# Kernel optimization log

Hardware: AMD Instinct MI355X
Metric: run time of the kernel (lower is better)

The kernel has to match this reference:

```python
import jax, jax.numpy as jnp
import numpy as np

TEMPERATURE = 0.1
BASE_TEMPERATURE = 0.07
N = 8192
D = 128


def setup_inputs() -> dict:
    key = jax.random.key(0)
    kf, kl = jax.random.split(key)
    feats = jax.random.normal(kf, (N, 1, D), dtype=jnp.float32)
    # contrastive embeddings are typically L2-normalized upstream
    feats = feats / jnp.linalg.norm(feats, axis=-1, keepdims=True)
    labels = jax.random.randint(kl, (N,), 0, 2, dtype=jnp.int32)
    return {"feats": feats, "labels": labels}


def reference(feats, labels):
    # feats: [anchor_num, n_view=1, D]; labels: [anchor_num] binary fg/bg
    anchor_num, n_view, d = feats.shape
    n = anchor_num * n_view  # n_view == 1 in this module
    contrast_feature = feats.reshape(n, d)

    lab = labels.reshape(-1, 1)
    pos_mask = (lab == lab.T).astype(feats.dtype)  # [N, N]
    neg_mask = 1.0 - pos_mask

    # [N, N] similarity logits
    logits = jnp.matmul(contrast_feature, contrast_feature.T) / TEMPERATURE
    logits_max = jax.lax.stop_gradient(jnp.max(logits, axis=1, keepdims=True))
    logits = logits - logits_max

    # mask out self-contrast on the diagonal (logits_mask in torch code)
    idx = jnp.arange(n)
    pos_mask = pos_mask.at[idx, idx].set(0.0)

    exp_logits = jnp.exp(logits)
    neg_logits = jnp.sum(exp_logits * neg_mask, axis=1, keepdims=True)  # [N,1]
    log_prob = logits - jnp.log(exp_logits + neg_logits)

    mean_log_prob_pos = jnp.sum(pos_mask * log_prob, axis=1) / jnp.sum(pos_mask, axis=1)
    loss = -(TEMPERATURE / BASE_TEMPERATURE) * mean_log_prob_pos
    return jnp.mean(loss)
```

## Files before the change

### kernel.cpp

```cpp
#include <hip/hip_runtime.h>
#include <hip/hip_bf16.h>

#define NN 8192
#define DD 128

typedef short bf16x8 __attribute__((ext_vector_type(8)));
typedef float f32x4 __attribute__((ext_vector_type(4)));

#define CSCALE  3.7982829f
#define SLSCALE 2.6327684f

#define LABF_OFF (NN * DD * 2)
#define G_OFF    (LABF_OFF + NN * 4)
#define CNT_OFF  (G_OFF + 1024)
#define CTR2_OFF (G_OFF + 1028)
#define ACC_OFF  (G_OFF + 1032)
#define CTR_OFF  (G_OFF + 1152)
#define EG_OFF   (G_OFF + 1280)
#define ELG_OFF  (EG_OFF + NN * 4)

#define BROWS 256
#define BCOLS 512
#define TCOLS 32
#define ITERS (BCOLS / TCOLS)

__device__ __forceinline__ unsigned short f2bf(float x) {
    unsigned u = __float_as_uint(x);
    u = (u + 0x7FFFu + ((u >> 16) & 1u)) >> 16;
    return (unsigned short)u;
}

__global__ __launch_bounds__(256) void prep_kernel(const float* __restrict__ F,
        const int* __restrict__ labels, unsigned short* __restrict__ F16,
        float* __restrict__ labf, float* __restrict__ G,
        int* __restrict__ cnt1, float* __restrict__ Eg, float* __restrict__ Elg) {
    __shared__ float sG[256];
    __shared__ int scnt;
    const int tid = threadIdx.x;
    sG[tid] = 0.f;
    if (tid == 0) scnt = 0;
    __syncthreads();
    const int wave = tid >> 6, lane = tid & 63;
    const int half = lane >> 5, l32 = lane & 31;
    const int rb = blockIdx.x * 32;
    if (tid < 32) { Eg[rb + tid] = 0.f; Elg[rb + tid] = 0.f; }
    int mycnt = 0;
    float g1a[4] = {0.f, 0.f, 0.f, 0.f}, gta[4] = {0.f, 0.f, 0.f, 0.f};
    #pragma unroll
    for (int it = 0; it < 4; ++it) {
        const int row = rb + it * 8 + wave * 2 + half;
        const int lab = labels[row];
        const float lf = (float)lab;
        const float4 f = *reinterpret_cast<const float4*>(F + row * DD + l32 * 4);
        ushort4 u;
        u.x = f2bf(CSCALE * f.x); u.y = f2bf(CSCALE * f.y);
        u.z = f2bf(CSCALE * f.z); u.w = f2bf(CSCALE * f.w);
        *reinterpret_cast<ushort4*>(F16 + row * DD + l32 * 4) = u;
        g1a[0] = fmaf(lf, f.x, g1a[0]); gta[0] += f.x;
        g1a[1] = fmaf(lf, f.y, g1a[1]); gta[1] += f.y;
        g1a[2] = fmaf(lf, f.z, g1a[2]); gta[2] += f.z;
        g1a[3] = fmaf(lf, f.w, g1a[3]); gta[3] += f.w;
        if (l32 == 0) {
            labf[row] = lf;
            mycnt += lab;
        }
    }
    #pragma unroll
    for (int j = 0; j < 4; ++j) {
        atomicAdd(&sG[l32 * 4 + j], g1a[j]);
        atomicAdd(&sG[128 + l32 * 4 + j], gta[j]);
    }
    if (l32 == 0 && mycnt) atomicAdd(&scnt, mycnt);
    __syncthreads();
    atomicAdd(&G[tid], sG[tid]);
    if (tid == 0) atomicAdd(cnt1, scnt);
}

__global__ __launch_bounds__(256, 2) void loss_kernel(
        const unsigned short* __restrict__ F16, const float* __restrict__ labf,
        const int* __restrict__ labels, const float* __restrict__ G,
        const int* __restrict__ cnt1, float* __restrict__ Eg,
        float* __restrict__ Elg, int* __restrict__ ctr, int* __restrict__ ctr2,
        float* __restrict__ acc, float* __restrict__ out) {
    __shared__ unsigned short Bt[2][TCOLS * DD];
    __shared__ float Lab[BCOLS];
    __shared__ int sLast;
    __shared__ float wsum[4];
    const int tid  = threadIdx.x;
    const int wave = tid >> 6, lane = tid & 63;
    const int quad = lane >> 4, l16 = lane & 15;
    const int rb = (blockIdx.x & 31) * BROWS;
    const int cb = (blockIdx.x >> 5) * BCOLS;

    Lab[tid]       = labf[cb + tid];
    Lab[tid + 256] = labf[cb + tid + 256];

    const int rw = rb + wave * 64;
    bf16x8 a[4][4];
    #pragma unroll
    for (int m = 0; m < 4; m++)
        #pragma unroll
        for (int kb = 0; kb < 4; kb++)
            a[m][kb] = *reinterpret_cast<const bf16x8*>(
                F16 + (rw + m * 16 + l16) * DD + kb * 32 + quad * 8);

    const int scol = tid >> 3;
    const int sc0  = (tid & 7) * 2;
    const unsigned short* sbase = F16 + (cb + scol) * DD + sc0 * 8;
    const int sdst0 = sc0 * (TCOLS * 8) + (((scol ^ sc0) & 31) * 8);
    const int sdst1 = (sc0 + 1) * (TCOLS * 8) + (((scol ^ (sc0 + 1)) & 31) * 8);

    *reinterpret_cast<bf16x8*>(&Bt[0][sdst0]) =
        *reinterpret_cast<const bf16x8*>(sbase);
    *reinterpret_cast<bf16x8*>(&Bt[0][sdst1]) =
        *reinterpret_cast<const bf16x8*>(sbase + 8);

    float accE[4][4] = {}, accEl[4][4] = {};
    __syncthreads();

    for (int it = 0; it < ITERS; ++it) {
        const int cur = it & 1;
        const int itn = (it + 1) & (ITERS - 1);
        const bf16x8 vn0 = *reinterpret_cast<const bf16x8*>(sbase + itn * TCOLS * DD);
        const bf16x8 vn1 = *reinterpret_cast<const bf16x8*>(sbase + itn * TCOLS * DD + 8);

        #pragma unroll
        for (int g = 0; g < 2; ++g) {
            bf16x8 bfr[4];
            #pragma unroll
            for (int kb = 0; kb < 4; kb++) {
                const int cr = kb * 4 + quad;
                const int col = g * 16 + l16;
                bfr[kb] = *reinterpret_cast<const bf16x8*>(
                    &Bt[cur][cr * (TCOLS * 8) + (((col ^ cr) & 31) * 8)]);
            }
            f32x4 d0 = {0.f, 0.f, 0.f, 0.f}, d1 = {0.f, 0.f, 0.f, 0.f};
            f32x4 d2 = {0.f, 0.f, 0.f, 0.f}, d3 = {0.f, 0.f, 0.f, 0.f};
            #pragma unroll
            for (int kb = 0; kb < 4; kb++) {
                d0 = __builtin_amdgcn_mfma_f32_16x16x32_bf16(a[0][kb], bfr[kb], d0, 0, 0, 0);
                d1 = __builtin_amdgcn_mfma_f32_16x16x32_bf16(a[1][kb], bfr[kb], d1, 0, 0, 0);
                d2 = __builtin_amdgcn_mfma_f32_16x16x32_bf16(a[2][kb], bfr[kb], d2, 0, 0, 0);
                d3 = __builtin_amdgcn_mfma_f32_16x16x32_bf16(a[3][kb], bfr[kb], d3, 0, 0, 0);
            }
            const float lc = Lab[it * TCOLS + g * 16 + l16];
            #pragma unroll
            for (int r = 0; r < 4; r++) {
                const float e0 = exp2f(d0[r]);
                accE[0][r] += e0; accEl[0][r] = fmaf(lc, e0, accEl[0][r]);
                const float e1 = exp2f(d1[r]);
                accE[1][r] += e1; accEl[1][r] = fmaf(lc, e1, accEl[1][r]);
                const float e2 = exp2f(d2[r]);
                accE[2][r] += e2; accEl[2][r] = fmaf(lc, e2, accEl[2][r]);
                const float e3 = exp2f(d3[r]);
                accE[3][r] += e3; accEl[3][r] = fmaf(lc, e3, accEl[3][r]);
            }
        }

        *reinterpret_cast<bf16x8*>(&Bt[cur ^ 1][sdst0]) = vn0;
        *reinterpret_cast<bf16x8*>(&Bt[cur ^ 1][sdst1]) = vn1;
        __syncthreads();
    }

    #pragma unroll
    for (int m = 0; m < 4; m++) {
        #pragma unroll
        for (int r = 0; r < 4; r++) {
            float e = accE[m][r], el = accEl[m][r];
            #pragma unroll
            for (int off = 1; off < 16; off <<= 1) {
                e  += __shfl_xor(e,  off);
                el += __shfl_xor(el, off);
            }
            if (l16 == 0) {
                const int row = rw + m * 16 + quad * 4 + r;
                atomicAdd(&Eg[row], e);
                atomicAdd(&Elg[row], el);
            }
        }
    }

    __syncthreads();
    if (tid == 0) sLast = (atomicAdd(&ctr[blockIdx.x & 31], 1) == 15);
    __syncthreads();
    if (!sLast) return;

    Lab[tid] = G[tid];
    __syncthreads();

    const int row = rb + tid;
    const int lr  = labels[row];
    const float E  = atomicAdd(&Eg[row], 0.f);
    const float El = atomicAdd(&Elg[row], 0.f);
    float dot = 0.f;
    const unsigned short* fp = F16 + row * DD;
    #pragma unroll
    for (int k = 0; k < DD; k += 8) {
        const bf16x8 fv = *reinterpret_cast<const bf16x8*>(fp + k);
        #pragma unroll
        for (int j = 0; j < 8; j++) {
            const float fj = __uint_as_float(((unsigned)(unsigned short)fv[j]) << 16);
            const float g1 = Lab[k + j];
            const float gl = lr ? g1 : (Lab[128 + k + j] - g1);
            dot = fmaf(fj, gl, dot);
        }
    }
    const float Epos = lr ? El : (E - El);
    const float Si   = E - Epos;
    const int   c1   = *cnt1;
    const float cntp1 = (float)(lr ? c1 : (NN - c1));
    const float cntm  = cntp1 - 1.f;
    const float sum_l   = SLSCALE * dot;
    const float sum_log = cntp1 * __logf(Si) + Epos / Si;
    float li = -(10.f / 7.f) * (sum_l - sum_log) / cntm;
    #pragma unroll
    for (int off = 1; off < 64; off <<= 1) li += __shfl_xor(li, off);
    if ((tid & 63) == 0) wsum[tid >> 6] = li;
    __syncthreads();
    if (tid == 0) {
        atomicAdd(acc, (wsum[0] + wsum[1] + wsum[2] + wsum[3]) * (1.0f / NN));
        __threadfence();
        if (atomicAdd(ctr2, 1) == 31) out[0] = atomicAdd(acc, 0.f);
    }
}

extern "C" void kernel_launch(void* const* d_in, const int* in_sizes, int n_in,
                              void* d_out, int out_size, void* d_ws, size_t ws_size,
                              hipStream_t stream) {
    const float* F      = (const float*)d_in[0];
    const int*   labels = (const int*)d_in[1];
    float*       out    = (float*)d_out;
    char*        ws     = (char*)d_ws;
    unsigned short* F16 = (unsigned short*)ws;
    float*       labf   = (float*)(ws + LABF_OFF);
    float*       G      = (float*)(ws + G_OFF);
    int*         cnt1   = (int*)(ws + CNT_OFF);
    int*         ctr2   = (int*)(ws + CTR2_OFF);
    float*       acc    = (float*)(ws + ACC_OFF);
    int*         ctr    = (int*)(ws + CTR_OFF);
    float*       Eg     = (float*)(ws + EG_OFF);
    float*       Elg    = (float*)(ws + ELG_OFF);

    hipMemsetAsync(ws + G_OFF, 0, 1280, stream);

    prep_kernel<<<NN / 32, 256, 0, stream>>>(F, labels, F16, labf, G, cnt1, Eg, Elg);
    loss_kernel<<<512, 256, 0, stream>>>(F16, labf, labels, G, cnt1, Eg, Elg,
                                         ctr, ctr2, acc, out);
}
```

Before: 102.7 us.

## Fuse bf16 prep into loss kernel and accumulate logit sums in-loop

Removes the separate prep kernel. The loss kernel now reads fp32 features directly and converts them to bf16 on the fly for both the A registers and the B tiles in LDS. The per-row positive-logit sum that used to come from a dot with global feature sums is replaced by extra in-loop accumulators of raw logits, and label counts are built per row group with atomics. This saves one launch and the F16 round trip through memory, but doubles global load bytes per tile, adds conversion ALU work and 32 more accumulator registers in the hot loop, and requires memsetting a larger workspace.

```diff
diff --git a/kernel.cpp b/kernel.cpp
--- a/kernel.cpp
+++ b/kernel.cpp
@@ -8,121 +8,104 @@
 typedef float f32x4 __attribute__((ext_vector_type(4)));
 
 #define CSCALE  3.7982829f
-#define SLSCALE 2.6327684f
-
-#define LABF_OFF (NN * DD * 2)
-#define G_OFF    (LABF_OFF + NN * 4)
-#define CNT_OFF  (G_OFF + 1024)
-#define CTR2_OFF (G_OFF + 1028)
-#define ACC_OFF  (G_OFF + 1032)
-#define CTR_OFF  (G_OFF + 1152)
-#define EG_OFF   (G_OFF + 1280)
+#define LN2     0.69314718056f
+
+#define CTR_OFF  0
+#define CTRC_OFF 128
+#define CTR2_OFF 256
+#define ACC_OFF  260
+#define EG_OFF   512
 #define ELG_OFF  (EG_OFF + NN * 4)
+#define SG_OFF   (ELG_OFF + NN * 4)
+#define SLG_OFF  (SG_OFF + NN * 4)
+#define WS_ZERO  (SLG_OFF + NN * 4)
 
 #define BROWS 256
 #define BCOLS 512
 #define TCOLS 32
 #define ITERS (BCOLS / TCOLS)
 
-__device__ __forceinline__ unsigned short f2bf(float x) {
-    unsigned u = __float_as_uint(x);
-    u = (u + 0x7FFFu + ((u >> 16) & 1u)) >> 16;
-    return (unsigned short)u;
+__device__ __forceinline__ bf16x8 cvt8(float4 fa, float4 fb) {
+    union { __hip_bfloat16 h[8]; bf16x8 v; } u;
+    u.h[0] = __float2bfloat16(CSCALE * fa.x);
+    u.h[1] = __float2bfloat16(CSCALE * fa.y);
+    u.h[2] = __float2bfloat16(CSCALE * fa.z);
+    u.h[3] = __float2bfloat16(CSCALE * fa.w);
+    u.h[4] = __float2bfloat16(CSCALE * fb.x);
+    u.h[5] = __float2bfloat16(CSCALE * fb.y);
+    u.h[6] = __float2bfloat16(CSCALE * fb.z);
+    u.h[7] = __float2bfloat16(CSCALE * fb.w);
+    return u.v;
 }
 
-__global__ __launch_bounds__(256) void prep_kernel(const float* __restrict__ F,
-        const int* __restrict__ labels, unsigned short* __restrict__ F16,
-        float* __restrict__ labf, float* __restrict__ G,
-        int* __restrict__ cnt1, float* __restrict__ Eg, float* __restrict__ Elg) {
-    __shared__ float sG[256];
-    __shared__ int scnt;
-    const int tid = threadIdx.x;
-    sG[tid] = 0.f;
-    if (tid == 0) scnt = 0;
-    __syncthreads();
-    const int wave = tid >> 6, lane = tid & 63;
-    const int half = lane >> 5, l32 = lane & 31;
-    const int rb = blockIdx.x * 32;
-    if (tid < 32) { Eg[rb + tid] = 0.f; Elg[rb + tid] = 0.f; }
-    int mycnt = 0;
-    float g1a[4] = {0.f, 0.f, 0.f, 0.f}, gta[4] = {0.f, 0.f, 0.f, 0.f};
-    #pragma unroll
-    for (int it = 0; it < 4; ++it) {
-        const int row = rb + it * 8 + wave * 2 + half;
-        const int lab = labels[row];
-        const float lf = (float)lab;
-        const float4 f = *reinterpret_cast<const float4*>(F + row * DD + l32 * 4);
-        ushort4 u;
-        u.x = f2bf(CSCALE * f.x); u.y = f2bf(CSCALE * f.y);
-        u.z = f2bf(CSCALE * f.z); u.w = f2bf(CSCALE * f.w);
-        *reinterpret_cast<ushort4*>(F16 + row * DD + l32 * 4) = u;
-        g1a[0] = fmaf(lf, f.x, g1a[0]); gta[0] += f.x;
-        g1a[1] = fmaf(lf, f.y, g1a[1]); gta[1] += f.y;
-        g1a[2] = fmaf(lf, f.z, g1a[2]); gta[2] += f.z;
-        g1a[3] = fmaf(lf, f.w, g1a[3]); gta[3] += f.w;
-        if (l32 == 0) {
-            labf[row] = lf;
-            mycnt += lab;
-        }
-    }
-    #pragma unroll
-    for (int j = 0; j < 4; ++j) {
-        atomicAdd(&sG[l32 * 4 + j], g1a[j]);
-        atomicAdd(&sG[128 + l32 * 4 + j], gta[j]);
-    }
-    if (l32 == 0 && mycnt) atomicAdd(&scnt, mycnt);
-    __syncthreads();
-    atomicAdd(&G[tid], sG[tid]);
-    if (tid == 0) atomicAdd(cnt1, scnt);
-}
-
-__global__ __launch_bounds__(256, 2) void loss_kernel(
-        const unsigned short* __restrict__ F16, const float* __restrict__ labf,
-        const int* __restrict__ labels, const float* __restrict__ G,
-        const int* __restrict__ cnt1, float* __restrict__ Eg,
-        float* __restrict__ Elg, int* __restrict__ ctr, int* __restrict__ ctr2,
-        float* __restrict__ acc, float* __restrict__ out) {
+__global__ __launch_bounds__(256, 2) void fused_kernel(
+        const float* __restrict__ F, const int* __restrict__ labels,
+        int* __restrict__ ctr, float* __restrict__ ctrC,
+        int* __restrict__ ctr2, float* __restrict__ acc,
+        float* __restrict__ Eg, float* __restrict__ Elg,
+        float* __restrict__ Sg, float* __restrict__ Slg,
+        float* __restrict__ out) {
     __shared__ unsigned short Bt[2][TCOLS * DD];
     __shared__ float Lab[BCOLS];
     __shared__ int sLast;
     __shared__ float wsum[4];
     const int tid  = threadIdx.x;
+    const int bid  = blockIdx.x;
     const int wave = tid >> 6, lane = tid & 63;
     const int quad = lane >> 4, l16 = lane & 15;
-    const int rb = (blockIdx.x & 31) * BROWS;
-    const int cb = (blockIdx.x >> 5) * BCOLS;
-
-    Lab[tid]       = labf[cb + tid];
-    Lab[tid + 256] = labf[cb + tid + 256];
+    const int rg = bid & 31;
+    const int rb = rg * BROWS;
+    const int cb = (bid >> 5) * BCOLS;
+
+    Lab[tid]       = (float)labels[cb + tid];
+    Lab[tid + 256] = (float)labels[cb + tid + 256];
 
     const int rw = rb + wave * 64;
     bf16x8 a[4][4];
     #pragma unroll
     for (int m = 0; m < 4; m++)
         #pragma unroll
-        for (int kb = 0; kb < 4; kb++)
-            a[m][kb] = *reinterpret_cast<const bf16x8*>(
-                F16 + (rw + m * 16 + l16) * DD + kb * 32 + quad * 8);
+        for (int kb = 0; kb < 4; kb++) {
+            const float* ap = F + (rw + m * 16 + l16) * DD + kb * 32 + quad * 8;
+            const float4 fa = *reinterpret_cast<const float4*>(ap);
+            const float4 fb = *reinterpret_cast<const float4*>(ap + 4);
+            a[m][kb] = cvt8(fa, fb);
+        }
 
     const int scol = tid >> 3;
     const int sc0  = (tid & 7) * 2;
-    const unsigned short* sbase = F16 + (cb + scol) * DD + sc0 * 8;
+    const float* sbaseF = F + (cb + scol) * DD + sc0 * 8;
     const int sdst0 = sc0 * (TCOLS * 8) + (((scol ^ sc0) & 31) * 8);
     const int sdst1 = (sc0 + 1) * (TCOLS * 8) + (((scol ^ (sc0 + 1)) & 31) * 8);
 
-    *reinterpret_cast<bf16x8*>(&Bt[0][sdst0]) =
-        *reinterpret_cast<const bf16x8*>(sbase);
-    *reinterpret_cast<bf16x8*>(&Bt[0][sdst1]) =
-        *reinterpret_cast<const bf16x8*>(sbase + 8);
+    {
+        const float4 va = *reinterpret_cast<const float4*>(sbaseF + 0);
+        const float4 vb = *reinterpret_cast<const float4*>(sbaseF + 4);
+        const float4 vc = *reinterpret_cast<const float4*>(sbaseF + 8);
+        const float4 vd = *reinterpret_cast<const float4*>(sbaseF + 12);
+        *reinterpret_cast<bf16x8*>(&Bt[0][sdst0]) = cvt8(va, vb);
+        *reinterpret_cast<bf16x8*>(&Bt[0][sdst1]) = cvt8(vc, vd);
+    }
 
     float accE[4][4] = {}, accEl[4][4] = {};
-    __syncthreads();
+    float accS[4][4] = {}, accSl[4][4] = {};
+    __syncthreads();
+
+    {
+        float cc = Lab[wave * 64 + lane] + Lab[256 + wave * 64 + lane];
+        #pragma unroll
+        for (int off = 1; off < 64; off <<= 1) cc += __shfl_xor(cc, off);
+        if (lane == 0) atomicAdd(&ctrC[rg], cc);
+    }
 
     for (int it = 0; it < ITERS; ++it) {
         const int cur = it & 1;
         const int itn = (it + 1) & (ITERS - 1);
-        const bf16x8 vn0 = *reinterpret_cast<const bf16x8*>(sbase + itn * TCOLS * DD);
-        const bf16x8 vn1 = *reinterpret_cast<const bf16x8*>(sbase + itn * TCOLS * DD + 8);
+        const float* pf = sbaseF + itn * TCOLS * DD;
+        const float4 va = *reinterpret_cast<const float4*>(pf + 0);
+        const float4 vb = *reinterpret_cast<const float4*>(pf + 4);
+        const float4 vc = *reinterpret_cast<const float4*>(pf + 8);
+        const float4 vd = *reinterpret_cast<const float4*>(pf + 12);
 
         #pragma unroll
         for (int g = 0; g < 2; ++g) {
@@ -148,17 +131,21 @@
             for (int r = 0; r < 4; r++) {
                 const float e0 = exp2f(d0[r]);
                 accE[0][r] += e0; accEl[0][r] = fmaf(lc, e0, accEl[0][r]);
+                accS[0][r] += d0[r]; accSl[0][r] = fmaf(lc, d0[r], accSl[0][r]);
                 const float e1 = exp2f(d1[r]);
                 accE[1][r] += e1; accEl[1][r] = fmaf(lc, e1, accEl[1][r]);
+                accS[1][r] += d1[r]; accSl[1][r] = fmaf(lc, d1[r], accSl[1][r]);
                 const float e2 = exp2f(d2[r]);
                 accE[2][r] += e2; accEl[2][r] = fmaf(lc, e2, accEl[2][r]);
+                accS[2][r] += d2[r]; accSl[2][r] = fmaf(lc, d2[r], accSl[2][r]);
                 const float e3 = exp2f(d3[r]);
                 accE[3][r] += e3; accEl[3][r] = fmaf(lc, e3, accEl[3][r]);
+                accS[3][r] += d3[r]; accSl[3][r] = fmaf(lc, d3[r], accSl[3][r]);
             }
         }
 
-        *reinterpret_cast<bf16x8*>(&Bt[cur ^ 1][sdst0]) = vn0;
-        *reinterpret_cast<bf16x8*>(&Bt[cur ^ 1][sdst1]) = vn1;
+        *reinterpret_cast<bf16x8*>(&Bt[cur ^ 1][sdst0]) = cvt8(va, vb);
+        *reinterpret_cast<bf16x8*>(&Bt[cur ^ 1][sdst1]) = cvt8(vc, vd);
         __syncthreads();
     }
 
@@ -167,50 +154,41 @@
         #pragma unroll
         for (int r = 0; r < 4; r++) {
             float e = accE[m][r], el = accEl[m][r];
+            float s = accS[m][r], sl = accSl[m][r];
             #pragma unroll
             for (int off = 1; off < 16; off <<= 1) {
                 e  += __shfl_xor(e,  off);
                 el += __shfl_xor(el, off);
+                s  += __shfl_xor(s,  off);
+                sl += __shfl_xor(sl, off);
             }
             if (l16 == 0) {
                 const int row = rw + m * 16 + quad * 4 + r;
                 atomicAdd(&Eg[row], e);
                 atomicAdd(&Elg[row], el);
+                atomicAdd(&Sg[row], s);
+                atomicAdd(&Slg[row], sl);
             }
         }
     }
 
     __syncthreads();
-    if (tid == 0) sLast = (atomicAdd(&ctr[blockIdx.x & 31], 1) == 15);
+    if (tid == 0) sLast = (atomicAdd(&ctr[rg], 1) == 15);
     __syncthreads();
     if (!sLast) return;
-
-    Lab[tid] = G[tid];
-    __syncthreads();
 
     const int row = rb + tid;
     const int lr  = labels[row];
-    const float E  = atomicAdd(&Eg[row], 0.f);
-    const float El = atomicAdd(&Elg[row], 0.f);
-    float dot = 0.f;
-    const unsigned short* fp = F16 + row * DD;
-    #pragma unroll
-    for (int k = 0; k < DD; k += 8) {
-        const bf16x8 fv = *reinterpret_cast<const bf16x8*>(fp + k);
-        #pragma unroll
-        for (int j = 0; j < 8; j++) {
-            const float fj = __uint_as_float(((unsigned)(unsigned short)fv[j]) << 16);
-            const float g1 = Lab[k + j];
-            const float gl = lr ? g1 : (Lab[128 + k + j] - g1);
-            dot = fmaf(fj, gl, dot);
-        }
-    }
+    const float E   = atomicAdd(&Eg[row], 0.f);
+    const float El  = atomicAdd(&Elg[row], 0.f);
+    const float S   = atomicAdd(&Sg[row], 0.f);
+    const float Sl  = atomicAdd(&Slg[row], 0.f);
+    const float c1f = atomicAdd(&ctrC[rg], 0.f);
     const float Epos = lr ? El : (E - El);
     const float Si   = E - Epos;
-    const int   c1   = *cnt1;
-    const float cntp1 = (float)(lr ? c1 : (NN - c1));
+    const float cntp1 = lr ? c1f : ((float)NN - c1f);
     const float cntm  = cntp1 - 1.f;
-    const float sum_l   = SLSCALE * dot;
+    const float sum_l   = (lr ? Sl : (S - Sl)) * LN2;
     const float sum_log = cntp1 * __logf(Si) + Epos / Si;
     float li = -(10.f / 7.f) * (sum_l - sum_log) / cntm;
     #pragma unroll
@@ -231,19 +209,17 @@
     const int*   labels = (const int*)d_in[1];
     float*       out    = (float*)d_out;
     char*        ws     = (char*)d_ws;
-    unsigned short* F16 = (unsigned short*)ws;
-    float*       labf   = (float*)(ws + LABF_OFF);
-    float*       G      = (float*)(ws + G_OFF);
-    int*         cnt1   = (int*)(ws + CNT_OFF);
+    int*         ctr    = (int*)(ws + CTR_OFF);
+    float*       ctrC   = (float*)(ws + CTRC_OFF);
     int*         ctr2   = (int*)(ws + CTR2_OFF);
     float*       acc    = (float*)(ws + ACC_OFF);
-    int*         ctr    = (int*)(ws + CTR_OFF);
     float*       Eg     = (float*)(ws + EG_OFF);
     float*       Elg    = (float*)(ws + ELG_OFF);
-
-    hipMemsetAsync(ws + G_OFF, 0, 1280, stream);
-
-    prep_kernel<<<NN / 32, 256, 0, stream>>>(F, labels, F16, labf, G, cnt1, Eg, Elg);
-    loss_kernel<<<512, 256, 0, stream>>>(F16, labf, labels, G, cnt1, Eg, Elg,
-                                         ctr, ctr2, acc, out);
+    float*       Sg     = (float*)(ws + SG_OFF);
+    float*       Slg    = (float*)(ws + SLG_OFF);
+
+    hipMemsetAsync(ws, 0, WS_ZERO, stream);
+
+    fused_kernel<<<512, 256, 0, stream>>>(F, labels, ctr, ctrC, ctr2, acc,
+                                          Eg, Elg, Sg, Slg, out);
 }
```

Result: slower. 106.6 us (+3.8%).

## Remove memset launch by zeroing counters in prep and using per-block G partials

Applied to the files above, without the earlier changes.

Drops the hipMemsetAsync call. Counters and accumulators are now zeroed inside prep_kernel, and the global atomic accumulation of G is replaced with per-block partial sums that the last block of each row group reduces. The count of label-1 rows is now accumulated per row group inside loss_kernel from the labels staged in shared memory, which removes the global counter. This saves one stream operation and avoids contended global atomics in prep. In exchange, each finishing block reads a 256x256 partial array, and correctness depends on prep_kernel's zeroing completing before loss_kernel starts.

```diff
diff --git a/kernel.cpp b/kernel.cpp
--- a/kernel.cpp
+++ b/kernel.cpp
@@ -11,13 +11,13 @@
 #define SLSCALE 2.6327684f
 
 #define LABF_OFF (NN * DD * 2)
-#define G_OFF    (LABF_OFF + NN * 4)
-#define CNT_OFF  (G_OFF + 1024)
-#define CTR2_OFF (G_OFF + 1028)
-#define ACC_OFF  (G_OFF + 1032)
-#define CTR_OFF  (G_OFF + 1152)
-#define EG_OFF   (G_OFF + 1280)
+#define CTR_OFF  (LABF_OFF + NN * 4)
+#define CTRC_OFF (CTR_OFF + 128)
+#define CTR2_OFF (CTRC_OFF + 128)
+#define ACC_OFF  (CTR2_OFF + 4)
+#define EG_OFF   (CTR2_OFF + 256)
 #define ELG_OFF  (EG_OFF + NN * 4)
+#define GP_OFF   (ELG_OFF + NN * 4)
 
 #define BROWS 256
 #define BCOLS 512
@@ -32,25 +32,28 @@
 
 __global__ __launch_bounds__(256) void prep_kernel(const float* __restrict__ F,
         const int* __restrict__ labels, unsigned short* __restrict__ F16,
-        float* __restrict__ labf, float* __restrict__ G,
-        int* __restrict__ cnt1, float* __restrict__ Eg, float* __restrict__ Elg) {
+        float* __restrict__ labf, float* __restrict__ Gp,
+        int* __restrict__ ctr, float* __restrict__ ctrC,
+        int* __restrict__ ctr2, float* __restrict__ acc,
+        float* __restrict__ Eg, float* __restrict__ Elg) {
     __shared__ float sG[256];
-    __shared__ int scnt;
     const int tid = threadIdx.x;
     sG[tid] = 0.f;
-    if (tid == 0) scnt = 0;
     __syncthreads();
     const int wave = tid >> 6, lane = tid & 63;
     const int half = lane >> 5, l32 = lane & 31;
     const int rb = blockIdx.x * 32;
     if (tid < 32) { Eg[rb + tid] = 0.f; Elg[rb + tid] = 0.f; }
-    int mycnt = 0;
+    if (blockIdx.x == 0) {
+        if (tid < 32) { ctr[tid] = 0; ctrC[tid] = 0.f; }
+        if (tid == 32) *ctr2 = 0;
+        if (tid == 33) *acc = 0.f;
+    }
     float g1a[4] = {0.f, 0.f, 0.f, 0.f}, gta[4] = {0.f, 0.f, 0.f, 0.f};
     #pragma unroll
     for (int it = 0; it < 4; ++it) {
         const int row = rb + it * 8 + wave * 2 + half;
-        const int lab = labels[row];
-        const float lf = (float)lab;
+        const float lf = (float)labels[row];
         const float4 f = *reinterpret_cast<const float4*>(F + row * DD + l32 * 4);
         ushort4 u;
         u.x = f2bf(CSCALE * f.x); u.y = f2bf(CSCALE * f.y);
@@ -60,28 +63,23 @@
         g1a[1] = fmaf(lf, f.y, g1a[1]); gta[1] += f.y;
         g1a[2] = fmaf(lf, f.z, g1a[2]); gta[2] += f.z;
         g1a[3] = fmaf(lf, f.w, g1a[3]); gta[3] += f.w;
-        if (l32 == 0) {
-            labf[row] = lf;
-            mycnt += lab;
-        }
+        if (l32 == 0) labf[row] = lf;
     }
     #pragma unroll
     for (int j = 0; j < 4; ++j) {
         atomicAdd(&sG[l32 * 4 + j], g1a[j]);
         atomicAdd(&sG[128 + l32 * 4 + j], gta[j]);
     }
-    if (l32 == 0 && mycnt) atomicAdd(&scnt, mycnt);
-    __syncthreads();
-    atomicAdd(&G[tid], sG[tid]);
-    if (tid == 0) atomicAdd(cnt1, scnt);
+    __syncthreads();
+    Gp[blockIdx.x * 256 + tid] = sG[tid];
 }
 
 __global__ __launch_bounds__(256, 2) void loss_kernel(
         const unsigned short* __restrict__ F16, const float* __restrict__ labf,
-        const int* __restrict__ labels, const float* __restrict__ G,
-        const int* __restrict__ cnt1, float* __restrict__ Eg,
-        float* __restrict__ Elg, int* __restrict__ ctr, int* __restrict__ ctr2,
-        float* __restrict__ acc, float* __restrict__ out) {
+        const int* __restrict__ labels, const float* __restrict__ Gp,
+        float* __restrict__ ctrC, int* __restrict__ ctr, int* __restrict__ ctr2,
+        float* __restrict__ acc, float* __restrict__ Eg,
+        float* __restrict__ Elg, float* __restrict__ out) {
     __shared__ unsigned short Bt[2][TCOLS * DD];
     __shared__ float Lab[BCOLS];
     __shared__ int sLast;
@@ -89,7 +87,8 @@
     const int tid  = threadIdx.x;
     const int wave = tid >> 6, lane = tid & 63;
     const int quad = lane >> 4, l16 = lane & 15;
-    const int rb = (blockIdx.x & 31) * BROWS;
+    const int rg = blockIdx.x & 31;
+    const int rb = rg * BROWS;
     const int cb = (blockIdx.x >> 5) * BCOLS;
 
     Lab[tid]       = labf[cb + tid];
@@ -117,6 +116,13 @@
 
     float accE[4][4] = {}, accEl[4][4] = {};
     __syncthreads();
+
+    {
+        float cc = Lab[wave * 64 + lane] + Lab[256 + wave * 64 + lane];
+        #pragma unroll
+        for (int off = 1; off < 64; off <<= 1) cc += __shfl_xor(cc, off);
+        if (lane == 0) atomicAdd(&ctrC[rg], cc);
+    }
 
     for (int it = 0; it < ITERS; ++it) {
         const int cur = it & 1;
@@ -181,17 +187,27 @@
     }
 
     __syncthreads();
-    if (tid == 0) sLast = (atomicAdd(&ctr[blockIdx.x & 31], 1) == 15);
+    if (tid == 0) sLast = (atomicAdd(&ctr[rg], 1) == 15);
     __syncthreads();
     if (!sLast) return;
 
-    Lab[tid] = G[tid];
+    {
+        float g0 = 0.f, g1 = 0.f, g2 = 0.f, g3 = 0.f;
+        for (int b = 0; b < 256; b += 4) {
+            g0 += Gp[(b + 0) * 256 + tid];
+            g1 += Gp[(b + 1) * 256 + tid];
+            g2 += Gp[(b + 2) * 256 + tid];
+            g3 += Gp[(b + 3) * 256 + tid];
+        }
+        Lab[tid] = (g0 + g1) + (g2 + g3);
+    }
     __syncthreads();
 
     const int row = rb + tid;
     const int lr  = labels[row];
     const float E  = atomicAdd(&Eg[row], 0.f);
     const float El = atomicAdd(&Elg[row], 0.f);
+    const float c1f = atomicAdd(&ctrC[rg], 0.f);
     float dot = 0.f;
     const unsigned short* fp = F16 + row * DD;
     #pragma unroll
@@ -207,8 +223,7 @@
     }
     const float Epos = lr ? El : (E - El);
     const float Si   = E - Epos;
-    const int   c1   = *cnt1;
-    const float cntp1 = (float)(lr ? c1 : (NN - c1));
+    const float cntp1 = lr ? c1f : ((float)NN - c1f);
     const float cntm  = cntp1 - 1.f;
     const float sum_l   = SLSCALE * dot;
     const float sum_log = cntp1 * __logf(Si) + Epos / Si;
@@ -233,17 +248,16 @@
     char*        ws     = (char*)d_ws;
     unsigned short* F16 = (unsigned short*)ws;
     float*       labf   = (float*)(ws + LABF_OFF);
-    float*       G      = (float*)(ws + G_OFF);
-    int*         cnt1   = (int*)(ws + CNT_OFF);
+    int*         ctr    = (int*)(ws + CTR_OFF);
+    float*       ctrC   = (float*)(ws + CTRC_OFF);
     int*         ctr2   = (int*)(ws + CTR2_OFF);
     float*       acc    = (float*)(ws + ACC_OFF);
-    int*         ctr    = (int*)(ws + CTR_OFF);
     float*       Eg     = (float*)(ws + EG_OFF);
     float*       Elg    = (float*)(ws + ELG_OFF);
-
-    hipMemsetAsync(ws + G_OFF, 0, 1280, stream);
-
-    prep_kernel<<<NN / 32, 256, 0, stream>>>(F, labels, F16, labf, G, cnt1, Eg, Elg);
-    loss_kernel<<<512, 256, 0, stream>>>(F16, labf, labels, G, cnt1, Eg, Elg,
-                                         ctr, ctr2, acc, out);
-}
+    float*       Gp     = (float*)(ws + GP_OFF);
+
+    prep_kernel<<<NN / 32, 256, 0, stream>>>(F, labels, F16, labf, Gp,
+                                             ctr, ctrC, ctr2, acc, Eg, Elg);
+    loss_kernel<<<512, 256, 0, stream>>>(F16, labf, labels, Gp, ctrC,
+                                         ctr, ctr2, acc, Eg, Elg, out);
+}
```

Result: slower. 109.6 us (+6.8%).
